# Kernel optimization log

Hardware: AMD Instinct MI355X
Metric: run time of the kernel (lower is better)

Reference implementation:

```python
import jax, jax.numpy as jnp
import numpy as np

MODES = 16

def _spectral_conv(x, w1r, w1i, w2r, w2i):
    # x: [N, Cin, R, R]; weights: [Cin, Cout, MODES, MODES] (real/imag parts)
    N, Cin, R, _ = x.shape
    Cout = w1r.shape[1]
    x_ft = jnp.fft.rfft2(x, axes=(-2, -1))  # [N, Cin, R, R//2+1] complex
    w1 = w1r + 1j * w1i
    w2 = w2r + 1j * w2i
    top = jnp.einsum('ncxy,coxy->noxy', x_ft[:, :, :MODES, :MODES], w1)
    bot = jnp.einsum('ncxy,coxy->noxy', x_ft[:, :, -MODES:, :MODES], w2)
    out_ft = jnp.zeros((N, Cout, R, R // 2 + 1), dtype=x_ft.dtype)
    out_ft = out_ft.at[:, :, :MODES, :MODES].set(top)
    out_ft = out_ft.at[:, :, -MODES:, :MODES].set(bot)
    return jnp.fft.irfft2(out_ft, s=(R, R), axes=(-2, -1))

def _forward(ref, w1r, w1i, w2r, w2i, subdomain_lookup):
    B, S, C, R, _ = ref.shape
    x = ref.reshape(B * S, C, R, R)
    # spectral conv + residual for ALL subdomains at once (vectorizes the torch loop)
    u_sub = _spectral_conv(x, w1r, w1i, w2r, w2i) + x  # [B*S, C, R, R]
    flat = u_sub.reshape(B, S, C, R * R)
    idx = subdomain_lookup.reshape(-1)  # [R*R], values in [0, S)
    pos = jnp.arange(R * R)
    # per-pixel select of owning subdomain: u[b, c, p] = flat[b, idx[p], c, p]
    # advanced indices (idx, pos) separated by a slice move to the front -> [R*R, B, C]
    u = flat[:, idx, :, pos]
    return jnp.transpose(u, (1, 2, 0)).reshape(B, C, R, R)

def setup_inputs():
    key = jax.random.key(0)
    ks = jax.random.split(key, 7)
    B, S, C, R, M = 4, 16, 64, 128, MODES
    scale = 1.0 / (C * C)
    return {
        'reference': jax.random.normal(ks[0], (B, S, C, R, R), dtype=jnp.float32),
        'physical_coords': jax.random.normal(ks[1], (2, R, R), dtype=jnp.float32),
        'subdomain_lookup': jax.random.randint(ks[2], (R, R), 0, S),
        'w1r': scale * jax.random.normal(ks[3], (C, C, M, M), dtype=jnp.float32),
        'w1i': scale * jax.random.normal(ks[4], (C, C, M, M), dtype=jnp.float32),
        'w2r': scale * jax.random.normal(ks[5], (C, C, M, M), dtype=jnp.float32),
        'w2i': scale * jax.random.normal(ks[6], (C, C, M, M), dtype=jnp.float32),
    }

def reference(reference, physical_coords, subdomain_lookup, w1r, w1i, w2r, w2i):
    del physical_coords  # only used for shape checks / dead ref_grid in the original
    return _forward(reference, w1r, w1i, w2r, w2i, subdomain_lookup)
```

## Files before the change

### kernel.cpp

```cpp
#include <hip/hip_runtime.h>
#include <math.h>


#define TWO_PI_OVER_128 0.04908738521234052f
#define RCAP 1280

typedef __attribute__((ext_vector_type(8))) short bf16x8;
typedef __attribute__((ext_vector_type(4))) float f32x4;
union FragU { uint4 u; bf16x8 s; };

__device__ __forceinline__ unsigned pk(float a, float b) {
  unsigned ua = __float_as_uint(a), ub = __float_as_uint(b);
  ua = (ua + 0x7FFFu + ((ua >> 16) & 1u)) >> 16;
  ub = (ub + 0x7FFFu + ((ub >> 16) & 1u)) >> 16;
  return ua | (ub << 16);
}
__device__ __forceinline__ float2 upk(unsigned v) {
  return make_float2(__uint_as_float(v << 16), __uint_as_float(v & 0xFFFF0000u));
}
__device__ __forceinline__ unsigned bf1(float a) {
  unsigned ua = __float_as_uint(a);
  return (ua + 0x7FFFu + ((ua >> 16) & 1u)) >> 16;
}

__global__ __launch_bounds__(1024) void kprep(const int* __restrict__ lu,
                                              int* __restrict__ scomb,
                                              int* __restrict__ plist,
                                              int* __restrict__ cntg,
                                              int* __restrict__ cnthg,
                                              unsigned* __restrict__ Etu,
                                              unsigned* __restrict__ Gtu,
                                              unsigned* __restrict__ G2tu,
                                              const float* __restrict__ w1r,
                                              const float* __restrict__ w1i,
                                              const float* __restrict__ w2r,
                                              const float* __restrict__ w2i,
                                              unsigned* __restrict__ Wt) {
  __shared__ int wsum[16];
  __shared__ unsigned tile[64 * 65];
  const int blk = blockIdx.x;
  const int tid = threadIdx.x;
  if (blk < 16) {
    const int s = blk;
    const int lane = tid & 63, wid = tid >> 6;
    const int4* lu4 = (const int4*)lu + tid * 4;
    unsigned match = 0;
#pragma unroll
    for (int q = 0; q < 4; ++q) {
      int4 v = lu4[q];
      match |= (v.x == s ? 1u : 0u) << (4 * q);
      match |= (v.y == s ? 1u : 0u) << (4 * q + 1);
      match |= (v.z == s ? 1u : 0u) << (4 * q + 2);
      match |= (v.w == s ? 1u : 0u) << (4 * q + 3);
    }
    const int cnt = __popc(match);
    int pre = cnt;
#pragma unroll
    for (int d = 1; d < 64; d <<= 1) {
      int t = __shfl_up(pre, d, 64);
      if (lane >= d) pre += t;
    }
    if (lane == 63) wsum[wid] = pre;
    __syncthreads();
    int woff = 0;
    for (int j = 0; j < wid; ++j) woff += wsum[j];
    int r = woff + pre - cnt;
    if (tid == 512) cnthg[s] = r;
    const int base = tid * 16;
#pragma unroll
    for (int i = 0; i < 16; ++i) {
      if ((match >> i) & 1u) {
        const int p = base + i;
        scomb[p] = (s << 12) | r;
        if (r < RCAP) plist[s * RCAP + r] = p;
        ++r;
      }
    }
    if (tid == 1023) {
      const int tot = woff + pre;
      cntg[s] = (tot < RCAP) ? tot : RCAP;
    }
  } else if (blk == 16) {
    for (int i = 0; i < 2; ++i) {
      int t = i * 1024 + tid;
      int w = t >> 6, y0 = (t & 63) * 2;
      float v[2];
#pragma unroll
      for (int q = 0; q < 2; ++q) {
        int y = y0 + q;
        if (w < 16) v[q] = cosf((float)((w * y) & 127) * TWO_PI_OVER_128);
        else        v[q] = -sinf((float)(((w - 16) * y) & 127) * TWO_PI_OVER_128);
      }
      Etu[t] = bf1(v[0]) | (bf1(v[1]) << 16);
    }
    for (int i = 0; i < 4; ++i) {
      int t = i * 1024 + tid;
      int jr = t >> 6, x0 = (t & 63) * 2;
      int j = (jr & 31);
      int kx = (j < 16) ? j : 96 + j;
      float v[2];
#pragma unroll
      for (int q = 0; q < 2; ++q) {
        int x = x0 + q;
        float a = (float)((kx * x) & 127) * TWO_PI_OVER_128;
        v[q] = (jr < 32) ? cosf(a) : sinf(a);
      }
      Gtu[t] = bf1(v[0]) | (bf1(v[1]) << 16);
    }
    for (int i = 0; i < 4; ++i) {
      int t = i * 1024 + tid;
      int x = t >> 5, k2 = t & 31;
      float v[2];
#pragma unroll
      for (int q = 0; q < 2; ++q) {
        int k = k2 * 2 + q;
        int kxi = k & 31;
        int kxe = (kxi < 16) ? kxi : 96 + kxi;
        float a = (float)((kxe * x) & 127) * TWO_PI_OVER_128;
        v[q] = (k < 32) ? cosf(a) : sinf(a);
      }
      G2tu[t] = bf1(v[0]) | (bf1(v[1]) << 16);
    }
  } else {
    const int ob = blk - 17;
    const int o = ob & 63, wsel = ob >> 6;
    const float* Wr = wsel ? w2r : w1r;
    const float* Wi = wsel ? w2i : w1i;
    for (int mc = 0; mc < 4; ++mc) {
      if (mc) __syncthreads();
      for (int i = 0; i < 4; ++i) {
        int idx = i * 1024 + tid;
        int c = idx >> 6, ml = idx & 63;
        int mh = mc * 64 + ml;
        float wsc = ((mh & 15) ? 2.f : 1.f) / 16384.f;
        size_t off = (size_t)(c * 64 + o) * 256 + mh;
        tile[c * 65 + ml] = pk(Wr[off] * wsc, Wi[off] * wsc);
      }
      __syncthreads();
      for (int i = 0; i < 4; ++i) {
        int idx = i * 1024 + tid;
        int ml = idx >> 6, c = idx & 63;
        Wt[(size_t)(wsel * 256 + mc * 64 + ml) * 4096 + o * 64 + c] = tile[c * 65 + ml];
      }
    }
  }
}

__global__ __launch_bounds__(256, 4) void k1_fwd(const float* __restrict__ ref,
                                                 const unsigned* __restrict__ Etu,
                                                 const unsigned* __restrict__ Gtu,
                                                 const int* __restrict__ cntg,
                                                 const int* __restrict__ cnthg,
                                                 const int* __restrict__ plist,
                                                 unsigned short* __restrict__ Rcomp,
                                                 unsigned* __restrict__ Xf) {
  __shared__ unsigned short imgL[64 * 128];
  __shared__ unsigned short A1t[2][32 * 128];
  unsigned* Xout = (unsigned*)imgL;
  const int bid2 = blockIdx.x;
  const int n = bid2 >> 5, cp = bid2 & 31;
  const int c0 = cp * 2;
  const int b = n >> 4, s = n & 15;
  const int tid = threadIdx.x;
  const int l = tid & 63, w = tid >> 6;

  FragU Ef[2][4];
#pragma unroll
  for (int nt = 0; nt < 2; ++nt)
#pragma unroll
    for (int ks = 0; ks < 4; ++ks)
      Ef[nt][ks].u = *(const uint4*)&Etu[(nt * 16 + (l & 15)) * 64 + ks * 16 + (l >> 4) * 4];

  const int ns = cntg[s], nh = cnthg[s];
  const int* pl = plist + s * RCAP;

  for (int img = 0; img < 2; ++img) {
    const int c = c0 + img;
    const float* imf = ref + (size_t)((n << 6) + c) * 16384;
    unsigned short* rc = Rcomp + ((size_t)((b << 6) + c) * 16 + s) * RCAP;
    for (int half = 0; half < 2; ++half) {
      if (img | half) __syncthreads();
      const float4* im4 = (const float4*)(imf + half * 8192);
      for (int i = 0; i < 8; ++i) {
        const int e4 = i * 256 + tid;
        float4 v = im4[e4];
        const int pl2 = e4 * 4;
        const int xl = pl2 >> 7, y0 = pl2 & 127;
        const int chunk = (y0 >> 3) ^ (xl & 15);
        *(uint2*)&imgL[xl * 128 + chunk * 8 + (y0 & 7)] =
            make_uint2(pk(v.x, v.y), pk(v.z, v.w));
      }
      __syncthreads();
      f32x4 acc1[2] = {};
      const int xl = w * 16 + (l & 15);
#pragma unroll
      for (int ks = 0; ks < 4; ++ks) {
        const int chunk = (ks * 4 + (l >> 4)) ^ (xl & 15);
        FragU a;
        a.u = *(const uint4*)&imgL[xl * 128 + chunk * 8];
#pragma unroll
        for (int nt = 0; nt < 2; ++nt)
          acc1[nt] = __builtin_amdgcn_mfma_f32_16x16x32_bf16(a.s, Ef[nt][ks].s, acc1[nt], 0, 0, 0);
      }
      {
        const int x0 = (half * 4 + w) * 16 + (l >> 4) * 4;
#pragma unroll
        for (int nt = 0; nt < 2; ++nt) {
          const int wp = nt * 16 + (l & 15);
          const int chunk = (x0 >> 3) ^ (wp & 15);
          *(uint2*)&A1t[img][wp * 128 + chunk * 8 + (x0 & 7)] =
              make_uint2(pk(acc1[nt][0], acc1[nt][1]), pk(acc1[nt][2], acc1[nt][3]));
        }
      }
      {
        const int rlo = half ? nh : 0, rhi = half ? ns : nh;
        for (int r = rlo + tid; r < rhi; r += 256) {
          const int p = pl[r];
          const int gxl = (p >> 7) - half * 64, y = p & 127;
          rc[r] = imgL[gxl * 128 + (((y >> 3) ^ (gxl & 15))) * 8 + (y & 7)];
        }
      }
    }
  }
  __syncthreads();

  {
    const int wi = w >> 1, wl = w & 1;
    FragU Gf[2];
    f32x4 acc2[2][2] = {};
#pragma unroll
    for (int ks = 0; ks < 4; ++ks) {
#pragma unroll
      for (int mtl = 0; mtl < 2; ++mtl)
        Gf[mtl].u = *(const uint4*)&Gtu[((wl + 2 * mtl) * 16 + (l & 15)) * 64 + ks * 16 + (l >> 4) * 4];
#pragma unroll
      for (int nt = 0; nt < 2; ++nt) {
        const int wp = nt * 16 + (l & 15);
        const int chunk = (ks * 4 + (l >> 4)) ^ (wp & 15);
        FragU bfr;
        bfr.u = *(const uint4*)&A1t[wi][wp * 128 + chunk * 8];
#pragma unroll
        for (int mtl = 0; mtl < 2; ++mtl)
          acc2[mtl][nt] = __builtin_amdgcn_mfma_f32_16x16x32_bf16(Gf[mtl].s, bfr.s, acc2[mtl][nt], 0, 0, 0);
      }
    }
#pragma unroll
    for (int r = 0; r < 4; ++r) {
      const int j = wl * 16 + (l >> 4) * 4 + r;
      const int ky = l & 15;
      const float re = acc2[0][0][r] + acc2[1][1][r];
      const float im = acc2[0][1][r] - acc2[1][0][r];
      Xout[wi * 512 + j * 16 + ky] = pk(re, im);
    }
  }
  __syncthreads();
  {
    uint2* dst = (uint2*)(Xf + (size_t)((n << 6) + c0) * 512);
    const uint2* src = (const uint2*)Xout;
    dst[tid] = src[tid];
    dst[tid + 256] = src[tid + 256];
  }
}

__global__ __launch_bounds__(256) void kt(const unsigned* __restrict__ Xf,
                                          unsigned* __restrict__ Xf2) {
  __shared__ unsigned tile[64 * 65];
  const int bm = blockIdx.x & 7, bn = blockIdx.x >> 3;
  const int tid = threadIdx.x;
  for (int i = 0; i < 16; ++i) {
    int idx = i * 256 + tid;
    int r = idx >> 6, cc = idx & 63;
    tile[r * 65 + cc] = Xf[(size_t)(bn * 64 + r) * 512 + bm * 64 + cc];
  }
  __syncthreads();
  for (int i = 0; i < 16; ++i) {
    int idx = i * 256 + tid;
    int r = idx >> 6, cc = idx & 63;
    Xf2[(size_t)(bm * 64 + r) * 4096 + bn * 64 + cc] = tile[cc * 65 + r];
  }
}

__global__ __launch_bounds__(256) void k2_mix(const unsigned* __restrict__ Xf2,
                                              const unsigned* __restrict__ Wt,
                                              unsigned* __restrict__ Yf) {
  __shared__ float2 Xs[64 * 65];
  __shared__ float2 Ws[64 * 65];
  const int m = blockIdx.x;
  const int tid = threadIdx.x;
  for (int i = 0; i < 16; ++i) {
    int e = i * 256 + tid;
    Xs[(e >> 6) * 65 + (e & 63)] = upk(Xf2[(size_t)m * 4096 + e]);
    Ws[(e >> 6) * 65 + (e & 63)] = upk(Wt[(size_t)m * 4096 + e]);
  }
  __syncthreads();
  const int g = tid >> 4, t = tid & 15;
  float accr[4][4] = {}, acci[4][4] = {};
  for (int cc = 0; cc < 64; ++cc) {
    float2 xv[4], wv[4];
#pragma unroll
    for (int k = 0; k < 4; ++k) xv[k] = Xs[(g + 16 * k) * 65 + cc];
#pragma unroll
    for (int j = 0; j < 4; ++j) wv[j] = Ws[(t + 16 * j) * 65 + cc];
#pragma unroll
    for (int k = 0; k < 4; ++k)
#pragma unroll
      for (int j = 0; j < 4; ++j) {
        accr[k][j] += xv[k].x * wv[j].x - xv[k].y * wv[j].y;
        acci[k][j] += xv[k].x * wv[j].y + xv[k].y * wv[j].x;
      }
  }
  __syncthreads();
  unsigned* Os = (unsigned*)Xs;
#pragma unroll
  for (int k = 0; k < 4; ++k)
#pragma unroll
    for (int j = 0; j < 4; ++j) {
      int bo = k * 64 + t + 16 * j;
      Os[bo * 17 + g] = pk(accr[k][j], acci[k][j]);
    }
  __syncthreads();
  for (int i = 0; i < 16; ++i) {
    int e = i * 256 + tid;
    int bo = e >> 4, ss = e & 15;
    Yf[(size_t)bo * 8192 + m * 16 + ss] = Os[bo * 17 + ss];
  }
}

__global__ __launch_bounds__(1024, 4) void k3_inv(const unsigned* __restrict__ Yf,
                                                  const unsigned* __restrict__ G2tu,
                                                  const int* __restrict__ scomb,
                                                  const unsigned short* __restrict__ Rcomp,
                                                  float* __restrict__ out) {
  __shared__ __align__(16) unsigned short Ypb[16 * 32 * 40];
  __shared__ __align__(16) unsigned short tbuf[16 * 546];
  __shared__ float2 tab[128];
  const int bo = blockIdx.x >> 1, half = blockIdx.x & 1;
  const int tid = threadIdx.x;
  const int l = tid & 63, w = tid >> 6;
  if (tid < 128) {
    float sv, cv;
    sincosf((float)tid * TWO_PI_OVER_128, &sv, &cv);
    tab[tid] = make_float2(cv, sv);
  }
  {
    const unsigned* src = Yf + (size_t)bo * 8192;
    for (int i = 0; i < 8; ++i) {
      int e = i * 1024 + tid;
      unsigned v = src[e];
      int ss = e & 15, m = e >> 4, kxi = m >> 4, ky = m & 15;
      unsigned short* yb = Ypb + ss * 1280;
      yb[ky * 40 + kxi] = (unsigned short)(v & 0xFFFFu);
      yb[(16 + ky) * 40 + kxi] = (unsigned short)(v >> 16);
    }
  }
  __syncthreads();
  float* outb = out + (size_t)bo * 16384;
  const unsigned short* rcb = Rcomp + (size_t)bo * 16 * RCAP;
  unsigned* tb32 = (unsigned*)tbuf;

  for (int ch = 0; ch < 4; ++ch) {
    const int xb = half * 64 + ch * 16;
    {
      const int xg = xb + (l & 15);
      FragU Ac, As, B0, B1;
      Ac.u = *(const uint4*)&G2tu[xg * 32 + (l >> 4) * 4];
      As.u = *(const uint4*)&G2tu[xg * 32 + 16 + (l >> 4) * 4];
      const unsigned short* yb = Ypb + w * 1280;
      B0.u = *(const uint4*)&yb[(l & 15) * 40 + (l >> 4) * 8];
      B1.u = *(const uint4*)&yb[(16 + (l & 15)) * 40 + (l >> 4) * 8];
      f32x4 z = {};
      f32x4 d1  = __builtin_amdgcn_mfma_f32_16x16x32_bf16(Ac.s, B0.s, z, 0, 0, 0);
      f32x4 d1b = __builtin_amdgcn_mfma_f32_16x16x32_bf16(Ac.s, B1.s, z, 0, 0, 0);
      f32x4 d2  = __builtin_amdgcn_mfma_f32_16x16x32_bf16(As.s, B0.s, z, 0, 0, 0);
      f32x4 d2b = __builtin_amdgcn_mfma_f32_16x16x32_bf16(As.s, B1.s, z, 0, 0, 0);
      const int ky = l & 15;
#pragma unroll
      for (int r = 0; r < 4; ++r) {
        const int xloc = (l >> 4) * 4 + r;
        tb32[w * 273 + xloc * 17 + ky] = pk(d1[r] - d2b[r], d1b[r] + d2[r]);
      }
    }
    __syncthreads();
    {
      const int xg = xb + w;
      const int pbase = xg * 128 + l * 2;
      const int2 sc2 = *(const int2*)&scomb[pbase];
      float o2[2];
#pragma unroll
      for (int q = 0; q < 2; ++q) {
        const int y = l * 2 + q;
        const int sc = q ? sc2.y : sc2.x;
        const int ssel = sc >> 12;
        const float rres = __uint_as_float((unsigned)rcb[ssel * RCAP + (sc & 4095)] << 16);
        const unsigned* tb = tb32 + ssel * 273 + w * 17;
        const float2 stpy = tab[y];
        float acc = 0.f, c0 = 1.f, s0 = 0.f;
#pragma unroll
        for (int k2 = 0; k2 < 16; ++k2) {
          const float2 tt = upk(tb[k2]);
          acc = fmaf(tt.x, c0, fmaf(-tt.y, s0, acc));
          float nc = c0 * stpy.x - s0 * stpy.y, ns = s0 * stpy.x + c0 * stpy.y;
          c0 = nc; s0 = ns;
        }
        o2[q] = rres + acc;
      }
      *(float2*)&outb[pbase] = make_float2(o2[0], o2[1]);
    }
    __syncthreads();
  }
}

extern "C" void kernel_launch(void* const* d_in, const int* in_sizes, int n_in,
                              void* d_out, int out_size, void* d_ws, size_t ws_size,
                              hipStream_t stream) {
  const float* ref = (const float*)d_in[0];
  const int* lu = (const int*)d_in[2];
  const float* w1r = (const float*)d_in[3];
  const float* w1i = (const float*)d_in[4];
  const float* w2r = (const float*)d_in[5];
  const float* w2i = (const float*)d_in[6];
  float* out = (float*)d_out;

  unsigned* Xf  = (unsigned*)d_ws;
  unsigned* Xf2 = Xf  + (size_t)4096 * 512;
  unsigned* Wt  = Xf2 + (size_t)4096 * 512;
  unsigned* Etu = Wt  + (size_t)4096 * 512;
  unsigned* Gtu = Etu + 2048;
  unsigned* G2tu = Gtu + 4096;
  int* cntg     = (int*)(G2tu + 4096);
  int* cnthg    = cntg + 16;
  int* plist    = cnthg + 16;
  int* scomb    = plist + 16 * RCAP;
  unsigned short* Rcomp = (unsigned short*)(scomb + 16384);
  unsigned* Yf  = Xf;

  kprep<<<145, 1024, 0, stream>>>(lu, scomb, plist, cntg, cnthg,
                                  Etu, Gtu, G2tu, w1r, w1i, w2r, w2i, Wt);
  k1_fwd<<<2048, 256, 0, stream>>>(ref, Etu, Gtu, cntg, cnthg, plist, Rcomp, Xf);
  kt<<<512, 256, 0, stream>>>(Xf, Xf2);
  k2_mix<<<512, 256, 0, stream>>>(Xf2, Wt, Yf);
  k3_inv<<<512, 1024, 0, stream>>>(Yf, G2tu, scomb, Rcomp, out);
}
```

Before: 129.3 us.

## Use bf16 MFMA for complex channel mixing with swizzled split real/imag LDS

Replaces the scalar FP32 complex multiply-accumulate in the channel-mixing kernel with four bf16 16x16x32 MFMA products per tile (rr, ii, ri, ir), which are combined into real and imaginary parts at the end. Inputs are unpacked into separate real and imaginary bf16 arrays in shared memory using an XOR swizzle to avoid bank conflicts. Output is written directly from registers as 16-byte vector stores, dropping the shared-memory transpose stage. The intent is to move the mixing FLOPs onto matrix cores; since inputs were already bf16, precision is only affected by accumulation order.

```diff
diff --git a/kernel.cpp b/kernel.cpp
--- a/kernel.cpp
+++ b/kernel.cpp
@@ -283,46 +283,56 @@
 __global__ __launch_bounds__(256) void k2_mix(const unsigned* __restrict__ Xf2,
                                               const unsigned* __restrict__ Wt,
                                               unsigned* __restrict__ Yf) {
-  __shared__ float2 Xs[64 * 65];
-  __shared__ float2 Ws[64 * 65];
+  __shared__ unsigned short Xr[64 * 64];
+  __shared__ unsigned short Xi[64 * 64];
+  __shared__ unsigned short Wr[64 * 64];
+  __shared__ unsigned short Wi[64 * 64];
   const int m = blockIdx.x;
   const int tid = threadIdx.x;
-  for (int i = 0; i < 16; ++i) {
-    int e = i * 256 + tid;
-    Xs[(e >> 6) * 65 + (e & 63)] = upk(Xf2[(size_t)m * 4096 + e]);
-    Ws[(e >> 6) * 65 + (e & 63)] = upk(Wt[(size_t)m * 4096 + e]);
+  const int l = tid & 63, w = tid >> 6;
+  for (int i = 0; i < 8; ++i) {
+    const int e0 = (i * 256 + tid) * 2;
+    const int n = e0 >> 6, cc = e0 & 63;
+    const int pos = n * 64 + (((cc >> 3) ^ (n & 7)) << 3) + (cc & 7);
+    uint2 xv = *(const uint2*)&Xf2[(size_t)m * 4096 + e0];
+    *(unsigned*)&Xr[pos] = (xv.x & 0xFFFFu) | (xv.y << 16);
+    *(unsigned*)&Xi[pos] = (xv.x >> 16) | (xv.y & 0xFFFF0000u);
+    uint2 wv = *(const uint2*)&Wt[(size_t)m * 4096 + e0];
+    *(unsigned*)&Wr[pos] = (wv.x & 0xFFFFu) | (wv.y << 16);
+    *(unsigned*)&Wi[pos] = (wv.x >> 16) | (wv.y & 0xFFFF0000u);
   }
   __syncthreads();
-  const int g = tid >> 4, t = tid & 15;
-  float accr[4][4] = {}, acci[4][4] = {};
-  for (int cc = 0; cc < 64; ++cc) {
-    float2 xv[4], wv[4];
-#pragma unroll
-    for (int k = 0; k < 4; ++k) xv[k] = Xs[(g + 16 * k) * 65 + cc];
-#pragma unroll
-    for (int j = 0; j < 4; ++j) wv[j] = Ws[(t + 16 * j) * 65 + cc];
-#pragma unroll
-    for (int k = 0; k < 4; ++k)
-#pragma unroll
-      for (int j = 0; j < 4; ++j) {
-        accr[k][j] += xv[k].x * wv[j].x - xv[k].y * wv[j].y;
-        acci[k][j] += xv[k].x * wv[j].y + xv[k].y * wv[j].x;
-      }
-  }
-  __syncthreads();
-  unsigned* Os = (unsigned*)Xs;
-#pragma unroll
-  for (int k = 0; k < 4; ++k)
-#pragma unroll
-    for (int j = 0; j < 4; ++j) {
-      int bo = k * 64 + t + 16 * j;
-      Os[bo * 17 + g] = pk(accr[k][j], acci[k][j]);
-    }
-  __syncthreads();
-  for (int i = 0; i < 16; ++i) {
-    int e = i * 256 + tid;
-    int bo = e >> 4, ss = e & 15;
-    Yf[(size_t)bo * 8192 + m * 16 + ss] = Os[bo * 17 + ss];
+  f32x4 acc[4][4] = {};
+  const int arow = w * 16 + (l & 15);
+#pragma unroll
+  for (int ks = 0; ks < 2; ++ks) {
+    FragU Ar, Ai;
+    {
+      const int chunk = ((ks * 4 + (l >> 4))) ^ (arow & 7);
+      Ar.u = *(const uint4*)&Xr[arow * 64 + chunk * 8];
+      Ai.u = *(const uint4*)&Xi[arow * 64 + chunk * 8];
+    }
+#pragma unroll
+    for (int nt = 0; nt < 4; ++nt) {
+      const int orow = nt * 16 + (l & 15);
+      const int chunk = ((ks * 4 + (l >> 4))) ^ (orow & 7);
+      FragU Br, Bi;
+      Br.u = *(const uint4*)&Wr[orow * 64 + chunk * 8];
+      Bi.u = *(const uint4*)&Wi[orow * 64 + chunk * 8];
+      acc[nt][0] = __builtin_amdgcn_mfma_f32_16x16x32_bf16(Ar.s, Br.s, acc[nt][0], 0, 0, 0);
+      acc[nt][1] = __builtin_amdgcn_mfma_f32_16x16x32_bf16(Ai.s, Bi.s, acc[nt][1], 0, 0, 0);
+      acc[nt][2] = __builtin_amdgcn_mfma_f32_16x16x32_bf16(Ar.s, Bi.s, acc[nt][2], 0, 0, 0);
+      acc[nt][3] = __builtin_amdgcn_mfma_f32_16x16x32_bf16(Ai.s, Br.s, acc[nt][3], 0, 0, 0);
+    }
+  }
+#pragma unroll
+  for (int nt = 0; nt < 4; ++nt) {
+    unsigned o4[4];
+#pragma unroll
+    for (int r = 0; r < 4; ++r)
+      o4[r] = pk(acc[nt][0][r] - acc[nt][1][r], acc[nt][2][r] + acc[nt][3][r]);
+    const int bo = w * 64 + nt * 16 + (l & 15);
+    *(uint4*)&Yf[(size_t)bo * 8192 + m * 16 + (l >> 4) * 4] = *(uint4*)o4;
   }
 }
 
```

Measured after the change: 113.1 us. 1.14x faster.
